# Kernel optimization log

Measured on AMD Instinct MI355X. Metric: run time of the kernel, lower is better.

The kernel has to match this reference:

```python
import jax, jax.numpy as jnp
import numpy as np

B, C_L_IN, C_L_OUT, C_J = 512, 64, 64, 16


def setup_inputs() -> dict:
    key = jax.random.key(0)
    ks = jax.random.split(key, 8)
    std = 0.02 / C_L_IN ** 0.5
    return {
        "F_in": jax.random.normal(ks[0], (B, C_L_IN, 4, 4), jnp.float32),
        "theta": jax.random.normal(ks[1], (B, C_J), jnp.float32),
        "W_bias": std * jax.random.normal(ks[2], (C_L_OUT, C_L_IN, 4, 4), jnp.float32),
        "W_cos": std * jax.random.normal(ks[3], (C_L_OUT, C_L_IN, C_J, 4, 4), jnp.float32),
        "W_sin": std * jax.random.normal(ks[4], (C_L_OUT, C_L_IN, C_J, 4, 4), jnp.float32),
        "Wb_bias": std * jax.random.normal(ks[5], (C_L_OUT, C_L_IN, 4, 4), jnp.float32),
        "Wb_cos": std * jax.random.normal(ks[6], (C_L_OUT, C_L_IN, C_J, 4, 4), jnp.float32),
        "Wb_sin": std * jax.random.normal(ks[7], (C_L_OUT, C_L_IN, C_J, 4, 4), jnp.float32),
    }


def reference(F_in, theta, W_bias, W_cos, W_sin, Wb_bias, Wb_cos, Wb_sin):
    cos_t = jnp.cos(theta)  # (B, C_J)
    sin_t = jnp.sin(theta)
    # U, Ub: (B, C_L_out, C_L_in, 4, 4)
    U = (W_bias
         + jnp.einsum('jicpq,bc->bjipq', W_cos, cos_t)
         + jnp.einsum('jicpq,bc->bjipq', W_sin, sin_t))
    Ub = (Wb_bias
          + jnp.einsum('jicpq,bc->bjipq', Wb_cos, cos_t)
          + jnp.einsum('jicpq,bc->bjipq', Wb_sin, sin_t))
    term1 = jnp.einsum('bipq,bjiqr->bjpr', F_in, U)
    term2 = jnp.einsum('bjipq,biqr->bjpr', Ub, F_in)
    return term1 + term2
```

## Files before the change

### kernel.cpp

```cpp
#include <hip/hip_runtime.h>


#define NRO_B   512
#define NRO_CL  64
#define K_DIM   8448
#define M_DIM   2048
#define N_DIM   256
#define SK      8
#define B_ELems  ((size_t)N_DIM * K_DIM)
#define FV_ELems ((size_t)M_DIM * N_DIM)
#define P_ELems  ((size_t)2 * SK * M_DIM * N_DIM)

typedef __attribute__((ext_vector_type(8))) _Float16 half8;
typedef __attribute__((ext_vector_type(4))) _Float16 half4_t;
typedef __attribute__((ext_vector_type(4))) float floatx4;

__device__ __forceinline__ void load16(const float* p, float w[4][4]) {
    const float4* p4 = (const float4*)p;
    #pragma unroll
    for (int a = 0; a < 4; ++a) {
        float4 x = p4[a];
        w[a][0] = x.x; w[a][1] = x.y; w[a][2] = x.z; w[a][3] = x.w;
    }
}

__device__ __forceinline__ half8 scale8(half8 v, _Float16 s) {
    half8 r;
    #pragma unroll
    for (int x = 0; x < 8; ++x) r[x] = v[x] * s;
    return r;
}

__global__ __launch_bounds__(256) void nro_prep(
    const float* __restrict__ F_in,
    const float* __restrict__ W_bias, const float* __restrict__ W_cos,
    const float* __restrict__ W_sin,  const float* __restrict__ Wb_bias,
    const float* __restrict__ Wb_cos, const float* __restrict__ Wb_sin,
    _Float16* __restrict__ Bbuf,
    _Float16* __restrict__ Fv)
{
    const int w = threadIdx.x >> 6, i = threadIdx.x & 63;
    if (blockIdx.x < 128) {
        const int b = blockIdx.x * 4 + w;
        float f[4][4];
        load16(F_in + ((size_t)b * 64 + i) * 16, f);
        #pragma unroll
        for (int a = 0; a < 4; ++a) {
            half4_t v0 = { (_Float16)f[a][0], (_Float16)f[a][1],
                           (_Float16)f[a][2], (_Float16)f[a][3] };
            *(half4_t*)(Fv + (size_t)(b * 4 + a) * 256 + i * 4) = v0;
            half4_t v1 = { (_Float16)f[0][a], (_Float16)f[1][a],
                           (_Float16)f[2][a], (_Float16)f[3][a] };
            *(half4_t*)(Fv + FV_ELems + (size_t)(b * 4 + a) * 256 + i * 4) = v1;
        }
    } else {
        const int unit = (blockIdx.x - 128) * 4 + w;
        const int j = unit >> 5, c = (unit >> 1) & 15, h = unit & 1;
        _Float16* Bd = Bbuf + (size_t)h * B_ELems;
        const size_t wbase = (((size_t)(j * 64 + i)) * 16 + c) * 16;

        float wc4[4][4], ws4[4][4];
        if (h == 0) { load16(W_cos  + wbase, wc4); load16(W_sin  + wbase, ws4); }
        else        { load16(Wb_cos + wbase, wc4); load16(Wb_sin + wbase, ws4); }

        #pragma unroll
        for (int a = 0; a < 4; ++a) {
            _Float16* n = Bd + (size_t)(j * 4 + a) * K_DIM + i * 4;
            half4_t vc, vs;
            if (h == 0) {
                vc = (half4_t){ (_Float16)wc4[0][a], (_Float16)wc4[1][a],
                                (_Float16)wc4[2][a], (_Float16)wc4[3][a] };
                vs = (half4_t){ (_Float16)ws4[0][a], (_Float16)ws4[1][a],
                                (_Float16)ws4[2][a], (_Float16)ws4[3][a] };
            } else {
                vc = (half4_t){ (_Float16)wc4[a][0], (_Float16)wc4[a][1],
                                (_Float16)wc4[a][2], (_Float16)wc4[a][3] };
                vs = (half4_t){ (_Float16)ws4[a][0], (_Float16)ws4[a][1],
                                (_Float16)ws4[a][2], (_Float16)ws4[a][3] };
            }
            *(half4_t*)(n + (1 + c)  * 256) = vc;
            *(half4_t*)(n + (17 + c) * 256) = vs;
        }
        if (c == 0) {
            float t[4][4];
            load16(((h == 0) ? W_bias : Wb_bias) + ((size_t)(j * 64 + i)) * 16, t);
            #pragma unroll
            for (int a = 0; a < 4; ++a) {
                half4_t v;
                if (h == 0) v = (half4_t){ (_Float16)t[0][a], (_Float16)t[1][a],
                                           (_Float16)t[2][a], (_Float16)t[3][a] };
                else        v = (half4_t){ (_Float16)t[a][0], (_Float16)t[a][1],
                                           (_Float16)t[a][2], (_Float16)t[a][3] };
                *(half4_t*)(Bd + (size_t)(j * 4 + a) * K_DIM + i * 4) = v;
            }
        }
    }
}

__global__ __launch_bounds__(256, 2) void nro_gemm(
    const _Float16* __restrict__ Bbuf, const _Float16* __restrict__ Fv,
    const float* __restrict__ theta,
    float* __restrict__ part)
{
    const int zs = blockIdx.x;
    const int z  = zs >> 3;
    const int sk = zs & 7;
    const int m0 = blockIdx.y * 64;

    const _Float16* Bm = Bbuf + (size_t)z * B_ELems;
    const _Float16* Fm = Fv + (size_t)z * FV_ELems + (size_t)m0 * 256;

    __shared__ _Float16 Fs[64 * 264];
    __shared__ _Float16 Bs[256 * 32];
    __shared__ float    trig[16 * 34];

    const int tid  = threadIdx.x;
    const int lane = tid & 63;
    const int w    = tid >> 6;
    const int wn   = w * 64;

    #pragma unroll
    for (int kk = 0; kk < 8; ++kk) {
        const int idx = kk * 256 + tid;
        const int row = idx >> 5, cf = idx & 31;
        half8 v = *(const half8*)(Fm + (size_t)row * 256 + cf * 8);
        *(half8*)(Fs + row * 264 + cf * 8) = v;
    }
    {
        const int bl = tid >> 4, c = tid & 15;
        const float th = theta[(m0 >> 2) * 16 + tid];
        trig[bl * 34 + 1 + c]  = __cosf(th);
        trig[bl * 34 + 17 + c] = __sinf(th);
        if (c == 0) trig[bl * 34] = 1.0f;
    }

    floatx4 acc[4][4] = {};
    const int rsub = lane >> 2, col8 = (lane & 3) * 8;
    const int fr = lane & 15,  fq = (lane >> 4) * 8;
    _Float16 tv[4] = {};

    for (int kt = 0; kt < 33; ++kt) {
        const int g   = sk * 33 + kt;
        const int cp  = g >> 3;
        const int iq0 = (g & 7) * 32;
        const int k0  = g * 32;
        __syncthreads();
        #pragma unroll
        for (int r = 0; r < 4; ++r) {
            const _Float16* gb = Bm + (size_t)(wn + r * 16 + rsub) * K_DIM + k0 + col8;
            __builtin_amdgcn_global_load_lds(
                (const __attribute__((address_space(1))) void*)gb,
                (__attribute__((address_space(3))) void*)(Bs + (wn + r * 16) * 32),
                16, 0, 0);
        }
        if (kt == 0 || (g & 7) == 0) {
            #pragma unroll
            for (int t = 0; t < 4; ++t)
                tv[t] = (_Float16)trig[(t * 4 + (fr >> 2)) * 34 + cp];
        }
        __syncthreads();

        half8 af[4], bf[4];
        #pragma unroll
        for (int t = 0; t < 4; ++t) {
            half8 fvf = *(const half8*)(Fs + (t * 16 + fr) * 264 + iq0 + fq);
            af[t] = scale8(fvf, tv[t]);
            bf[t] = *(const half8*)(Bs + (wn + t * 16 + fr) * 32 + fq);
        }
        #pragma unroll
        for (int mt = 0; mt < 4; ++mt)
            #pragma unroll
            for (int nt = 0; nt < 4; ++nt)
                acc[mt][nt] = __builtin_amdgcn_mfma_f32_16x16x32_f16(
                    af[mt], bf[nt], acc[mt][nt], 0, 0, 0);
    }

    const int col = lane & 15, row4 = (lane >> 4) * 4;
    #pragma unroll
    for (int mt = 0; mt < 4; ++mt)
        #pragma unroll
        for (int nt = 0; nt < 4; ++nt)
            #pragma unroll
            for (int e = 0; e < 4; ++e) {
                const int m = m0 + mt * 16 + row4 + e;
                const int n = wn + nt * 16 + col;
                part[((size_t)zs * M_DIM + m) * N_DIM + n] = acc[mt][nt][e];
            }
}

__global__ __launch_bounds__(256) void nro_reduce(
    const float* __restrict__ part, float* __restrict__ out)
{
    const int t = blockIdx.x * 256 + threadIdx.x;
    const int b = t >> 8;
    const int j = (t >> 2) & 63;
    const int p = t & 3;

    float4 o = make_float4(0.f, 0.f, 0.f, 0.f);
    #pragma unroll
    for (int sk = 0; sk < SK; ++sk) {
        const float4 c1 = *(const float4*)(
            part + ((size_t)sk * M_DIM + b * 4 + p) * N_DIM + j * 4);
        o.x += c1.x; o.y += c1.y; o.z += c1.z; o.w += c1.w;
        const float* p2 = part + ((size_t)(SK + sk) * M_DIM + b * 4) * N_DIM + j * 4 + p;
        o.x += p2[0 * N_DIM]; o.y += p2[1 * N_DIM];
        o.z += p2[2 * N_DIM]; o.w += p2[3 * N_DIM];
    }
    *(float4*)(out + ((size_t)(b * 64 + j) * 16 + p * 4)) = o;
}

__global__ __launch_bounds__(256, 2) void nro_fallback(
    const float* __restrict__ F_in, const float* __restrict__ theta,
    const float* __restrict__ W_bias, const float* __restrict__ W_cos,
    const float* __restrict__ W_sin,  const float* __restrict__ Wb_bias,
    const float* __restrict__ Wb_cos, const float* __restrict__ Wb_sin,
    float* __restrict__ out)
{
    __shared__ float smem[8448];
    const int j      = blockIdx.x >> 3;
    const int isplit = blockIdx.x & 7;
    const int i0     = isplit * 8;
    const int lane   = threadIdx.x & 63;
    const int chunk  = __builtin_amdgcn_readfirstlane(threadIdx.x >> 6);
    const int b      = blockIdx.y * 64 + lane;
    const int tid    = threadIdx.x;
    {
        float4* s4 = (float4*)smem;
        const int base16  = (j * 64 + i0) * 16;
        const int base256 = (j * 64 + i0) * 256;
        if (tid < 32)      s4[tid] = ((const float4*)(W_bias + base16))[tid];
        else if (tid < 64) s4[tid] = ((const float4*)(Wb_bias + base16))[tid - 32];
        #pragma unroll
        for (int r = 0; r < 2; ++r) {
            const int k = r * 256 + tid;
            s4[64 + k]   = ((const float4*)(W_cos  + base256))[k];
            s4[576 + k]  = ((const float4*)(W_sin  + base256))[k];
            s4[1088 + k] = ((const float4*)(Wb_cos + base256))[k];
            s4[1600 + k] = ((const float4*)(Wb_sin + base256))[k];
        }
    }
    float csc[16], css[16];
    #pragma unroll
    for (int c = 0; c < 16; ++c) {
        float t = theta[b * 16 + c];
        csc[c] = __cosf(t); css[c] = __sinf(t);
    }
    __syncthreads();
    float acc[16];
    #pragma unroll
    for (int e = 0; e < 16; ++e) acc[e] = 0.0f;
    #pragma unroll
    for (int ii = 0; ii < 2; ++ii) {
        const int il = chunk * 2 + ii;
        const int i  = i0 + il;
        float f[16];
        const float4* fp = (const float4*)(F_in + (b * 64 + i) * 16);
        #pragma unroll
        for (int v = 0; v < 4; ++v) {
            float4 x = fp[v];
            f[v*4+0]=x.x; f[v*4+1]=x.y; f[v*4+2]=x.z; f[v*4+3]=x.w;
        }
        const float* wb  = smem + il * 16;
        const float* wbb = smem + 128  + il * 16;
        const float* wc  = smem + 256  + il * 256;
        const float* wsn = smem + 2304 + il * 256;
        const float* wbc = smem + 4352 + il * 256;
        const float* wbs = smem + 6400 + il * 256;
        float U[16], Ub[16];
        #pragma unroll
        for (int e = 0; e < 16; ++e) { U[e] = wb[e]; Ub[e] = wbb[e]; }
        #pragma unroll 4
        for (int c = 0; c < 16; ++c) {
            const float cc = csc[c], ss = css[c];
            #pragma unroll
            for (int e = 0; e < 16; ++e) {
                U[e]  = fmaf(wc [c*16+e], cc, U[e]);
                U[e]  = fmaf(wsn[c*16+e], ss, U[e]);
                Ub[e] = fmaf(wbc[c*16+e], cc, Ub[e]);
                Ub[e] = fmaf(wbs[c*16+e], ss, Ub[e]);
            }
        }
        #pragma unroll
        for (int p = 0; p < 4; ++p)
            #pragma unroll
            for (int r = 0; r < 4; ++r) {
                float a = acc[p*4+r];
                #pragma unroll
                for (int q = 0; q < 4; ++q) {
                    a = fmaf(f[p*4+q],  U[q*4+r], a);
                    a = fmaf(Ub[p*4+q], f[q*4+r], a);
                }
                acc[p*4+r] = a;
            }
    }
    __syncthreads();
    if (chunk > 0) {
        float* r = smem + (chunk - 1) * 1088 + lane * 17;
        #pragma unroll
        for (int e = 0; e < 16; ++e) r[e] = acc[e];
    }
    __syncthreads();
    if (chunk == 0) {
        #pragma unroll
        for (int cc = 0; cc < 3; ++cc) {
            const float* r = smem + cc * 1088 + lane * 17;
            #pragma unroll
            for (int e = 0; e < 16; ++e) acc[e] += r[e];
        }
        float* o = out + ((size_t)b * 64 + j) * 16;
        #pragma unroll
        for (int e = 0; e < 16; ++e) atomicAdd(o + e, acc[e]);
    }
}

extern "C" void kernel_launch(void* const* d_in, const int* in_sizes, int n_in,
                              void* d_out, int out_size, void* d_ws, size_t ws_size,
                              hipStream_t stream) {
    const float* F_in    = (const float*)d_in[0];
    const float* theta   = (const float*)d_in[1];
    const float* W_bias  = (const float*)d_in[2];
    const float* W_cos   = (const float*)d_in[3];
    const float* W_sin   = (const float*)d_in[4];
    const float* Wb_bias = (const float*)d_in[5];
    const float* Wb_cos  = (const float*)d_in[6];
    const float* Wb_sin  = (const float*)d_in[7];
    float* out = (float*)d_out;

    const size_t needB  = 2 * B_ELems  * sizeof(_Float16);
    const size_t needFv = 2 * FV_ELems * sizeof(_Float16);
    const size_t needP  = P_ELems * sizeof(float);
    if (ws_size >= needB + needFv + needP) {
        _Float16* Bbuf = (_Float16*)d_ws;
        _Float16* Fv   = (_Float16*)((char*)d_ws + needB);
        float*    part = (float*)((char*)d_ws + needB + needFv);
        nro_prep<<<640, 256, 0, stream>>>(F_in, W_bias, W_cos, W_sin,
                                          Wb_bias, Wb_cos, Wb_sin, Bbuf, Fv);
        nro_gemm<<<dim3(16, 32), 256, 0, stream>>>(Bbuf, Fv, theta, part);
        nro_reduce<<<512, 256, 0, stream>>>(part, out);
    } else {
        hipMemsetAsync(out, 0, (size_t)out_size * sizeof(float), stream);
        dim3 grid(64 * 8, 512 / 64, 1);
        nro_fallback<<<grid, 256, 0, stream>>>(
            F_in, theta, W_bias, W_cos, W_sin, Wb_bias, Wb_cos, Wb_sin, out);
    }
}
```

Baseline: 115.0 us.

## Load B fragments directly from global into registers with one-step prefetch

Drops the LDS staging buffer for B. Each wave now reads its own B fragments straight from global memory into registers and prefetches the next k-step while the current MFMAs run. This removes two block-wide barriers per k-iteration and the LDS round trip, since each wave uses only its own B rows. In exchange the global loads are less coalesced (16-byte reads scattered across rows) and register pressure goes up.

```diff
diff --git a/kernel.cpp b/kernel.cpp
--- a/kernel.cpp
+++ b/kernel.cpp
@@ -111,7 +111,6 @@
     const _Float16* Fm = Fv + (size_t)z * FV_ELems + (size_t)m0 * 256;
 
     __shared__ _Float16 Fs[64 * 264];
-    __shared__ _Float16 Bs[256 * 32];
     __shared__ float    trig[16 * 34];
 
     const int tid  = threadIdx.x;
@@ -133,39 +132,44 @@
         trig[bl * 34 + 17 + c] = __sinf(th);
         if (c == 0) trig[bl * 34] = 1.0f;
     }
+    __syncthreads();
+
+    const int fr = lane & 15, fq = (lane >> 4) * 8;
+
+    const _Float16* Brow[4];
+    #pragma unroll
+    for (int t = 0; t < 4; ++t)
+        Brow[t] = Bm + (size_t)(wn + t * 16 + fr) * K_DIM + fq;
 
     floatx4 acc[4][4] = {};
-    const int rsub = lane >> 2, col8 = (lane & 3) * 8;
-    const int fr = lane & 15,  fq = (lane >> 4) * 8;
     _Float16 tv[4] = {};
 
-    for (int kt = 0; kt < 33; ++kt) {
-        const int g   = sk * 33 + kt;
+    int g = sk * 33;
+    half8 bf[4];
+    #pragma unroll
+    for (int t = 0; t < 4; ++t) bf[t] = *(const half8*)(Brow[t] + g * 32);
+
+    for (int kt = 0; kt < 33; ++kt, ++g) {
         const int cp  = g >> 3;
         const int iq0 = (g & 7) * 32;
-        const int k0  = g * 32;
-        __syncthreads();
-        #pragma unroll
-        for (int r = 0; r < 4; ++r) {
-            const _Float16* gb = Bm + (size_t)(wn + r * 16 + rsub) * K_DIM + k0 + col8;
-            __builtin_amdgcn_global_load_lds(
-                (const __attribute__((address_space(1))) void*)gb,
-                (__attribute__((address_space(3))) void*)(Bs + (wn + r * 16) * 32),
-                16, 0, 0);
-        }
         if (kt == 0 || (g & 7) == 0) {
             #pragma unroll
             for (int t = 0; t < 4; ++t)
                 tv[t] = (_Float16)trig[(t * 4 + (fr >> 2)) * 34 + cp];
         }
-        __syncthreads();
-
-        half8 af[4], bf[4];
+        half8 bn[4];
+        #pragma unroll
+        for (int t = 0; t < 4; ++t) bn[t] = bf[t];
+        if (kt < 32) {
+            #pragma unroll
+            for (int t = 0; t < 4; ++t)
+                bn[t] = *(const half8*)(Brow[t] + (g + 1) * 32);
+        }
+        half8 af[4];
         #pragma unroll
         for (int t = 0; t < 4; ++t) {
             half8 fvf = *(const half8*)(Fs + (t * 16 + fr) * 264 + iq0 + fq);
             af[t] = scale8(fvf, tv[t]);
-            bf[t] = *(const half8*)(Bs + (wn + t * 16 + fr) * 32 + fq);
         }
         #pragma unroll
         for (int mt = 0; mt < 4; ++mt)
@@ -173,6 +177,8 @@
             for (int nt = 0; nt < 4; ++nt)
                 acc[mt][nt] = __builtin_amdgcn_mfma_f32_16x16x32_f16(
                     af[mt], bf[nt], acc[mt][nt], 0, 0, 0);
+        #pragma unroll
+        for (int t = 0; t < 4; ++t) bf[t] = bn[t];
     }
 
     const int col = lane & 15, row4 = (lane >> 4) * 4;
```

After: 124.4 us. 8.1% more time.
